# Kernel optimization log

Measured on AMD Instinct MI355X. Metric: run time of the kernel, lower is better.

The kernel has to match this reference:

```python
import jax, jax.numpy as jnp
import numpy as np

NUM_TYPES = 100
D_MODEL = 256
EPS = 1e-5


def setup_inputs() -> dict:
    key = jax.random.key(0)
    ks = jax.random.split(key, 8)
    N = 524288
    z = jax.random.randint(ks[0], (N,), 0, NUM_TYPES)
    x = jax.random.normal(ks[1], (N, 3), dtype=jnp.float32)
    emb = jax.random.normal(ks[2], (NUM_TYPES, D_MODEL), dtype=jnp.float32)
    w1 = jax.random.normal(ks[3], (3, D_MODEL), dtype=jnp.float32) * (1.0 / np.sqrt(3.0))
    b1 = jnp.zeros((D_MODEL,), dtype=jnp.float32)
    w2 = jax.random.normal(ks[4], (D_MODEL, D_MODEL), dtype=jnp.float32) * (1.0 / np.sqrt(D_MODEL))
    b2 = jnp.zeros((D_MODEL,), dtype=jnp.float32)
    gamma = jnp.ones((D_MODEL,), dtype=jnp.float32)
    beta = jnp.zeros((D_MODEL,), dtype=jnp.float32)
    return {"z": z, "x": x, "emb": emb, "w1": w1, "b1": b1,
            "w2": w2, "b2": b2, "gamma": gamma, "beta": beta}


def reference(z, x, emb, w1, b1, w2, b2, gamma, beta):
    # Embedding gather: [N, d]
    h = emb[z]
    # pos MLP: Linear(3,d) -> SiLU -> Linear(d,d)
    p = jnp.dot(x, w1) + b1
    p = jax.nn.silu(p)
    p = jnp.dot(p, w2) + b2
    h = h + p
    # LayerNorm over last dim
    mu = jnp.mean(h, axis=-1, keepdims=True)
    var = jnp.mean(jnp.square(h - mu), axis=-1, keepdims=True)
    h = (h - mu) * jax.lax.rsqrt(var + EPS) * gamma + beta
    return h
```

## Files before the change

### kernel.cpp

```cpp
#include <hip/hip_runtime.h>

#define EPS 1e-5f
#define WAVES 4

typedef __attribute__((ext_vector_type(8)))  short short8;
typedef __attribute__((ext_vector_type(4)))  short short4_t;
typedef __attribute__((ext_vector_type(16))) float f32x16;
typedef __attribute__((ext_vector_type(4)))  float f32x4;

__device__ inline unsigned f2bf(float f) {
    unsigned u = __builtin_bit_cast(unsigned, f);
    return (u + 0x7fffu + ((u >> 16) & 1u)) >> 16;
}

__global__ void prep(const float* __restrict__ w2, const float* __restrict__ emb,
                     const float* __restrict__ b2,
                     unsigned short* __restrict__ w2f, unsigned* __restrict__ embp) {
    int idx = blockIdx.x * 256 + threadIdx.x;
    if (idx < 65536) {
        int e    = idx & 7;
        int lane = (idx >> 3) & 63;
        int ks   = (idx >> 9) & 15;
        int nf   = idx >> 13;
        int k    = ks * 16 + ((lane >> 5) << 3) + e;
        int n    = nf * 32 + (lane & 31);
        w2f[idx] = (unsigned short)f2bf(w2[k * 256 + n]);
    } else if (idx < 65536 + 12800) {
        int i   = idx - 65536;
        int row = i >> 7;
        int w   = i & 127;
        int g   = w >> 5;
        int c   = w & 31;
        int clo = g * 64 + c;
        int chi = clo + 32;
        unsigned lo = f2bf(emb[row * 256 + clo] + b2[clo]);
        unsigned hi = f2bf(emb[row * 256 + chi] + b2[chi]);
        embp[i] = lo | (hi << 16);
    }
}

__global__ __launch_bounds__(256, 2) void fused_kernel(
    const int* __restrict__ z, const float* __restrict__ x,
    const float* __restrict__ w1, const float* __restrict__ b1,
    const unsigned short* __restrict__ w2f, const unsigned* __restrict__ embp,
    const float* __restrict__ gamma, const float* __restrict__ beta,
    float* __restrict__ out, int N)
{
    __shared__ char  p_lds[WAVES * 16384];
    __shared__ float x_lds[WAVES][32][4];
    __shared__ int   z_lds[WAVES][32];

    const int tid  = threadIdx.x;
    const int wave = tid >> 6;
    const int lane = tid & 63;
    const int l31  = lane & 31;
    const int h    = lane >> 5;
    char* pbuf = p_lds + wave * 16384;

    const int tiles = N >> 5;
    const int t = blockIdx.x * WAVES + wave;
    if (t >= tiles) return;
    const int R = t << 5;

    if (lane < 32) {
        int r = R + lane;
        x_lds[wave][lane][0] = x[r * 3 + 0];
        x_lds[wave][lane][1] = x[r * 3 + 1];
        x_lds[wave][lane][2] = x[r * 3 + 2];
        z_lds[wave][lane]    = z[r];
    }

    f32x16 acc[8];
#pragma unroll
    for (int j = 0; j < 16; ++j) {
        const int rl = (j & 3) + ((j >> 2) << 3) + (h << 2);
        const unsigned* er = embp + z_lds[wave][rl] * 128 + l31;
#pragma unroll
        for (int g = 0; g < 4; ++g) {
            unsigned u = er[g * 32];
            acc[2 * g][j]     = __builtin_bit_cast(float, u << 16);
            acc[2 * g + 1][j] = __builtin_bit_cast(float, u & 0xffff0000u);
        }
    }

    const int  c0  = lane * 4;
    const f32x4 w1a = *(const f32x4*)(w1 + c0);
    const f32x4 w1b = *(const f32x4*)(w1 + 256 + c0);
    const f32x4 w1c = *(const f32x4*)(w1 + 512 + c0);
    const f32x4 b1v = *(const f32x4*)(b1 + c0);
    float gv[8], bv[8];
#pragma unroll
    for (int nf = 0; nf < 8; ++nf) {
        int c = nf * 32 + l31;
        gv[nf] = gamma[c]; bv[nf] = beta[c];
    }

#pragma unroll
    for (int r = 0; r < 32; ++r) {
        float x0 = x_lds[wave][r][0];
        float x1 = x_lds[wave][r][1];
        float x2 = x_lds[wave][r][2];
        short4_t pv;
#pragma unroll
        for (int j = 0; j < 4; ++j) {
            float tv = x0 * w1a[j] + x1 * w1b[j] + x2 * w1c[j] + b1v[j];
            float s  = tv * __builtin_amdgcn_rcpf(1.f + __expf(-tv));
            pv[j] = (short)f2bf(s);
        }
        int off = (r * 512 + lane * 8) ^ ((r & 7) << 4);
        *(short4_t*)(pbuf + off) = pv;
    }

#pragma unroll
    for (int ks = 0; ks < 16; ++ks) {
        int aoff = (l31 * 512 + ks * 32 + h * 16) ^ ((l31 & 7) << 4);
        short8 a = *(const short8*)(pbuf + aoff);
        const unsigned short* bp = w2f + ks * 512 + lane * 8;
#pragma unroll
        for (int nf = 0; nf < 8; ++nf) {
            short8 b = *(const short8*)(bp + nf * 8192);
            acc[nf] = __builtin_amdgcn_mfma_f32_32x32x16_bf16(a, b, acc[nf], 0, 0, 0);
        }
    }

#pragma unroll
    for (int j = 0; j < 16; ++j) {
        const int rl = (j & 3) + ((j >> 2) << 3) + (h << 2);
        float hv[8];
        float hsum = 0.f, hsq = 0.f;
#pragma unroll
        for (int nf = 0; nf < 8; ++nf) {
            float v = acc[nf][j];
            hv[nf] = v; hsum += v; hsq += v * v;
        }
#pragma unroll
        for (int d = 1; d < 32; d <<= 1) {
            hsum += __shfl_xor(hsum, d, 64);
            hsq  += __shfl_xor(hsq,  d, 64);
        }
        float mu  = hsum * (1.f / 256.f);
        float var = hsq * (1.f / 256.f) - mu * mu;
        float rs  = rsqrtf(var + EPS);
        float* orow = out + (size_t)(R + rl) * 256 + l31;
#pragma unroll
        for (int nf = 0; nf < 8; ++nf)
            __builtin_nontemporal_store((hv[nf] - mu) * rs * gv[nf] + bv[nf],
                                        orow + nf * 32);
    }
}

extern "C" void kernel_launch(void* const* d_in, const int* in_sizes, int n_in,
                              void* d_out, int out_size, void* d_ws, size_t ws_size,
                              hipStream_t stream) {
    const int*   z     = (const int*)d_in[0];
    const float* x     = (const float*)d_in[1];
    const float* emb   = (const float*)d_in[2];
    const float* w1    = (const float*)d_in[3];
    const float* b1    = (const float*)d_in[4];
    const float* w2    = (const float*)d_in[5];
    const float* b2    = (const float*)d_in[6];
    const float* gamma = (const float*)d_in[7];
    const float* beta  = (const float*)d_in[8];
    float* out = (float*)d_out;
    const int N = in_sizes[0];

    unsigned short* w2f  = (unsigned short*)d_ws;
    unsigned*       embp = (unsigned*)((char*)d_ws + 131072);

    prep<<<(65536 + 12800 + 255) / 256, 256, 0, stream>>>(w2, emb, b2, w2f, embp);

    int tiles  = N >> 5;
    int blocks = (tiles + WAVES - 1) / WAVES;
    fused_kernel<<<blocks, 256, 0, stream>>>(z, x, w1, b1, w2f, embp,
                                             gamma, beta, out, N);
}
```

Before: 185.0 us.

## Split output columns across waves with shared 64-row A tile and cross-wave LayerNorm

The block now handles 64 rows instead of one 32-row tile per wave. Each of the four waves computes 64 output columns for all 64 rows, so the SiLU activation tile is built once in LDS and shared, and each wave loads only a quarter of W2. The accumulator count drops from 8 to 4 MFMA tiles per wave, which lowers register pressure and lets launch bounds ask for 3 blocks per CU. The cost is extra __syncthreads barriers and a cross-wave LDS reduction of the LayerNorm partial sums.

```diff
diff --git a/kernel.cpp b/kernel.cpp
--- a/kernel.cpp
+++ b/kernel.cpp
@@ -1,7 +1,6 @@
 #include <hip/hip_runtime.h>
 
 #define EPS 1e-5f
-#define WAVES 4
 
 typedef __attribute__((ext_vector_type(8)))  short short8;
 typedef __attribute__((ext_vector_type(4)))  short short4_t;
@@ -39,67 +38,66 @@
     }
 }
 
-__global__ __launch_bounds__(256, 2) void fused_kernel(
+__global__ __launch_bounds__(256, 3) void fused_kernel(
     const int* __restrict__ z, const float* __restrict__ x,
     const float* __restrict__ w1, const float* __restrict__ b1,
     const unsigned short* __restrict__ w2f, const unsigned* __restrict__ embp,
     const float* __restrict__ gamma, const float* __restrict__ beta,
     float* __restrict__ out, int N)
 {
-    __shared__ char  p_lds[WAVES * 16384];
-    __shared__ float x_lds[WAVES][32][4];
-    __shared__ int   z_lds[WAVES][32];
+    __shared__ char  a_lds[32768];
+    __shared__ float x_lds[64][4];
+    __shared__ int   z_lds[64];
+    __shared__ float part[64][4][2];
 
     const int tid  = threadIdx.x;
     const int wave = tid >> 6;
     const int lane = tid & 63;
     const int l31  = lane & 31;
     const int h    = lane >> 5;
-    char* pbuf = p_lds + wave * 16384;
+    const int l15  = lane & 15;
+    const int h4   = lane >> 4;
 
-    const int tiles = N >> 5;
-    const int t = blockIdx.x * WAVES + wave;
-    if (t >= tiles) return;
-    const int R = t << 5;
+    const int R = blockIdx.x << 6;
 
-    if (lane < 32) {
-        int r = R + lane;
-        x_lds[wave][lane][0] = x[r * 3 + 0];
-        x_lds[wave][lane][1] = x[r * 3 + 1];
-        x_lds[wave][lane][2] = x[r * 3 + 2];
-        z_lds[wave][lane]    = z[r];
+    if (tid < 64) {
+        int r = R + tid;
+        x_lds[tid][0] = x[r * 3 + 0];
+        x_lds[tid][1] = x[r * 3 + 1];
+        x_lds[tid][2] = x[r * 3 + 2];
+        z_lds[tid]    = z[r];
+    }
+    __syncthreads();
+
+    f32x16 acc[2][2];
+#pragma unroll
+    for (int rb = 0; rb < 2; ++rb)
+#pragma unroll
+    for (int j = 0; j < 16; ++j) {
+        const int row = rb * 32 + (j & 3) + ((j >> 2) << 3) + (h << 2);
+        unsigned u = embp[z_lds[row] * 128 + wave * 32 + l31];
+        acc[rb][0][j] = __builtin_bit_cast(float, u << 16);
+        acc[rb][1][j] = __builtin_bit_cast(float, u & 0xffff0000u);
     }
 
-    f32x16 acc[8];
+    float gv[2], bv[2];
 #pragma unroll
-    for (int j = 0; j < 16; ++j) {
-        const int rl = (j & 3) + ((j >> 2) << 3) + (h << 2);
-        const unsigned* er = embp + z_lds[wave][rl] * 128 + l31;
-#pragma unroll
-        for (int g = 0; g < 4; ++g) {
-            unsigned u = er[g * 32];
-            acc[2 * g][j]     = __builtin_bit_cast(float, u << 16);
-            acc[2 * g + 1][j] = __builtin_bit_cast(float, u & 0xffff0000u);
-        }
+    for (int nfi = 0; nfi < 2; ++nfi) {
+        int c = wave * 64 + nfi * 32 + l31;
+        gv[nfi] = gamma[c]; bv[nfi] = beta[c];
     }
 
-    const int  c0  = lane * 4;
+    const int  c0  = wave * 64 + l15 * 4;
     const f32x4 w1a = *(const f32x4*)(w1 + c0);
     const f32x4 w1b = *(const f32x4*)(w1 + 256 + c0);
     const f32x4 w1c = *(const f32x4*)(w1 + 512 + c0);
     const f32x4 b1v = *(const f32x4*)(b1 + c0);
-    float gv[8], bv[8];
 #pragma unroll
-    for (int nf = 0; nf < 8; ++nf) {
-        int c = nf * 32 + l31;
-        gv[nf] = gamma[c]; bv[nf] = beta[c];
-    }
-
-#pragma unroll
-    for (int r = 0; r < 32; ++r) {
-        float x0 = x_lds[wave][r][0];
-        float x1 = x_lds[wave][r][1];
-        float x2 = x_lds[wave][r][2];
+    for (int rr = 0; rr < 16; ++rr) {
+        const int row = h4 * 16 + rr;
+        float x0 = x_lds[row][0];
+        float x1 = x_lds[row][1];
+        float x2 = x_lds[row][2];
         short4_t pv;
 #pragma unroll
         for (int j = 0; j < 4; ++j) {
@@ -107,45 +105,57 @@
             float s  = tv * __builtin_amdgcn_rcpf(1.f + __expf(-tv));
             pv[j] = (short)f2bf(s);
         }
-        int off = (r * 512 + lane * 8) ^ ((r & 7) << 4);
-        *(short4_t*)(pbuf + off) = pv;
+        int off = (row * 512 + c0 * 2) ^ ((row & 7) << 4);
+        *(short4_t*)(a_lds + off) = pv;
+    }
+    __syncthreads();
+
+#pragma unroll
+    for (int ks = 0; ks < 16; ++ks) {
+        short8 a0 = *(const short8*)(a_lds + ((l31 * 512 + ks * 32 + h * 16) ^ ((l31 & 7) << 4)));
+        short8 a1 = *(const short8*)(a_lds + (((32 + l31) * 512 + ks * 32 + h * 16) ^ ((l31 & 7) << 4)));
+        const unsigned short* bp = w2f + ks * 512 + lane * 8;
+        short8 b0 = *(const short8*)(bp + (2 * wave) * 8192);
+        short8 b1f = *(const short8*)(bp + (2 * wave + 1) * 8192);
+        acc[0][0] = __builtin_amdgcn_mfma_f32_32x32x16_bf16(a0, b0,  acc[0][0], 0, 0, 0);
+        acc[0][1] = __builtin_amdgcn_mfma_f32_32x32x16_bf16(a0, b1f, acc[0][1], 0, 0, 0);
+        acc[1][0] = __builtin_amdgcn_mfma_f32_32x32x16_bf16(a1, b0,  acc[1][0], 0, 0, 0);
+        acc[1][1] = __builtin_amdgcn_mfma_f32_32x32x16_bf16(a1, b1f, acc[1][1], 0, 0, 0);
     }
 
 #pragma unroll
-    for (int ks = 0; ks < 16; ++ks) {
-        int aoff = (l31 * 512 + ks * 32 + h * 16) ^ ((l31 & 7) << 4);
-        short8 a = *(const short8*)(pbuf + aoff);
-        const unsigned short* bp = w2f + ks * 512 + lane * 8;
+    for (int rb = 0; rb < 2; ++rb)
 #pragma unroll
-        for (int nf = 0; nf < 8; ++nf) {
-            short8 b = *(const short8*)(bp + nf * 8192);
-            acc[nf] = __builtin_amdgcn_mfma_f32_32x32x16_bf16(a, b, acc[nf], 0, 0, 0);
+    for (int j = 0; j < 16; ++j) {
+        float s = acc[rb][0][j] + acc[rb][1][j];
+        float q = acc[rb][0][j] * acc[rb][0][j] + acc[rb][1][j] * acc[rb][1][j];
+#pragma unroll
+        for (int d = 1; d < 32; d <<= 1) {
+            s += __shfl_xor(s, d, 64);
+            q += __shfl_xor(q, d, 64);
         }
+        const int row = rb * 32 + (j & 3) + ((j >> 2) << 3) + (h << 2);
+        if (l31 == 0) { part[row][wave][0] = s; part[row][wave][1] = q; }
     }
+    __syncthreads();
 
 #pragma unroll
+    for (int rb = 0; rb < 2; ++rb)
+#pragma unroll
     for (int j = 0; j < 16; ++j) {
-        const int rl = (j & 3) + ((j >> 2) << 3) + (h << 2);
-        float hv[8];
-        float hsum = 0.f, hsq = 0.f;
+        const int row = rb * 32 + (j & 3) + ((j >> 2) << 3) + (h << 2);
+        f32x4 p0 = *(const f32x4*)&part[row][0][0];
+        f32x4 p1 = *(const f32x4*)&part[row][2][0];
+        float sum = p0[0] + p0[2] + p1[0] + p1[2];
+        float sq  = p0[1] + p0[3] + p1[1] + p1[3];
+        float mu  = sum * (1.f / 256.f);
+        float var = sq * (1.f / 256.f) - mu * mu;
+        float rs  = rsqrtf(var + EPS);
+        float* orow = out + (size_t)(R + row) * 256 + wave * 64 + l31;
 #pragma unroll
-        for (int nf = 0; nf < 8; ++nf) {
-            float v = acc[nf][j];
-            hv[nf] = v; hsum += v; hsq += v * v;
-        }
-#pragma unroll
-        for (int d = 1; d < 32; d <<= 1) {
-            hsum += __shfl_xor(hsum, d, 64);
-            hsq  += __shfl_xor(hsq,  d, 64);
-        }
-        float mu  = hsum * (1.f / 256.f);
-        float var = hsq * (1.f / 256.f) - mu * mu;
-        float rs  = rsqrtf(var + EPS);
-        float* orow = out + (size_t)(R + rl) * 256 + l31;
-#pragma unroll
-        for (int nf = 0; nf < 8; ++nf)
-            __builtin_nontemporal_store((hv[nf] - mu) * rs * gv[nf] + bv[nf],
-                                        orow + nf * 32);
+        for (int nfi = 0; nfi < 2; ++nfi)
+            __builtin_nontemporal_store((acc[rb][nfi][j] - mu) * rs * gv[nfi] + bv[nfi],
+                                        orow + nfi * 32);
     }
 }
 
@@ -169,8 +179,7 @@
 
     prep<<<(65536 + 12800 + 255) / 256, 256, 0, stream>>>(w2, emb, b2, w2f, embp);
 
-    int tiles  = N >> 5;
-    int blocks = (tiles + WAVES - 1) / WAVES;
+    int blocks = N >> 6;
     fused_kernel<<<blocks, 256, 0, stream>>>(z, x, w1, b1, w2f, embp,
                                              gamma, beta, out, N);
 }
```

New measurement: 223.7 us. 20.9% more time.

## Split hidden-dim SiLU and GEMM into two halves to halve LDS buffer

Applied to the files above, without the earlier changes.

The first-layer SiLU output is now produced and consumed in two 128-column halves, each followed by its 8 K-steps of MFMA, so the per-wave LDS staging buffer shrinks from 16KB to 8KB. This cuts LDS per block from 64KB to 32KB, which may allow more resident blocks per CU and lets SiLU compute of one half interleave with MFMA work. In exchange there is an extra phase boundary per tile, and occupancy may still be capped by registers (launch_bounds 256,2).

```diff
diff --git a/kernel.cpp b/kernel.cpp
--- a/kernel.cpp
+++ b/kernel.cpp
@@ -4,9 +4,8 @@
 #define WAVES 4
 
 typedef __attribute__((ext_vector_type(8)))  short short8;
-typedef __attribute__((ext_vector_type(4)))  short short4_t;
 typedef __attribute__((ext_vector_type(16))) float f32x16;
-typedef __attribute__((ext_vector_type(4)))  float f32x4;
+typedef __attribute__((ext_vector_type(2)))  float f32x2;
 
 __device__ inline unsigned f2bf(float f) {
     unsigned u = __builtin_bit_cast(unsigned, f);
@@ -46,7 +45,7 @@
     const float* __restrict__ gamma, const float* __restrict__ beta,
     float* __restrict__ out, int N)
 {
-    __shared__ char  p_lds[WAVES * 16384];
+    __shared__ char  p_lds[WAVES * 8192];
     __shared__ float x_lds[WAVES][32][4];
     __shared__ int   z_lds[WAVES][32];
 
@@ -55,7 +54,7 @@
     const int lane = tid & 63;
     const int l31  = lane & 31;
     const int h    = lane >> 5;
-    char* pbuf = p_lds + wave * 16384;
+    char* pbuf = p_lds + wave * 8192;
 
     const int tiles = N >> 5;
     const int t = blockIdx.x * WAVES + wave;
@@ -83,46 +82,45 @@
         }
     }
 
-    const int  c0  = lane * 4;
-    const f32x4 w1a = *(const f32x4*)(w1 + c0);
-    const f32x4 w1b = *(const f32x4*)(w1 + 256 + c0);
-    const f32x4 w1c = *(const f32x4*)(w1 + 512 + c0);
-    const f32x4 b1v = *(const f32x4*)(b1 + c0);
+#pragma unroll
+    for (int half = 0; half < 2; ++half) {
+        const int c = half * 128 + lane * 2;
+        const f32x2 wa = *(const f32x2*)(w1 + c);
+        const f32x2 wb = *(const f32x2*)(w1 + 256 + c);
+        const f32x2 wc = *(const f32x2*)(w1 + 512 + c);
+        const f32x2 bb = *(const f32x2*)(b1 + c);
+#pragma unroll
+        for (int r = 0; r < 32; ++r) {
+            float x0 = x_lds[wave][r][0];
+            float x1 = x_lds[wave][r][1];
+            float x2 = x_lds[wave][r][2];
+            float t0 = x0 * wa[0] + x1 * wb[0] + x2 * wc[0] + bb[0];
+            float t1 = x0 * wa[1] + x1 * wb[1] + x2 * wc[1] + bb[1];
+            float s0 = t0 * __builtin_amdgcn_rcpf(1.f + __expf(-t0));
+            float s1 = t1 * __builtin_amdgcn_rcpf(1.f + __expf(-t1));
+            unsigned pv = f2bf(s0) | (f2bf(s1) << 16);
+            int off = (r * 256 + lane * 4) ^ ((r & 7) << 4);
+            *(unsigned*)(pbuf + off) = pv;
+        }
+#pragma unroll
+        for (int ks = 0; ks < 8; ++ks) {
+            int aoff = (l31 * 256 + ks * 32 + h * 16) ^ ((l31 & 7) << 4);
+            short8 a = *(const short8*)(pbuf + aoff);
+            const unsigned short* bp = w2f + (half * 8 + ks) * 512 + lane * 8;
+#pragma unroll
+            for (int nf = 0; nf < 8; ++nf) {
+                short8 b = *(const short8*)(bp + nf * 8192);
+                acc[nf] = __builtin_amdgcn_mfma_f32_32x32x16_bf16(a, b, acc[nf], 0, 0, 0);
+            }
+        }
+    }
+
     float gv[8], bv[8];
 #pragma unroll
     for (int nf = 0; nf < 8; ++nf) {
-        int c = nf * 32 + l31;
-        gv[nf] = gamma[c]; bv[nf] = beta[c];
+        int cc = nf * 32 + l31;
+        gv[nf] = gamma[cc]; bv[nf] = beta[cc];
     }
-
-#pragma unroll
-    for (int r = 0; r < 32; ++r) {
-        float x0 = x_lds[wave][r][0];
-        float x1 = x_lds[wave][r][1];
-        float x2 = x_lds[wave][r][2];
-        short4_t pv;
-#pragma unroll
-        for (int j = 0; j < 4; ++j) {
-            float tv = x0 * w1a[j] + x1 * w1b[j] + x2 * w1c[j] + b1v[j];
-            float s  = tv * __builtin_amdgcn_rcpf(1.f + __expf(-tv));
-            pv[j] = (short)f2bf(s);
-        }
-        int off = (r * 512 + lane * 8) ^ ((r & 7) << 4);
-        *(short4_t*)(pbuf + off) = pv;
-    }
-
-#pragma unroll
-    for (int ks = 0; ks < 16; ++ks) {
-        int aoff = (l31 * 512 + ks * 32 + h * 16) ^ ((l31 & 7) << 4);
-        short8 a = *(const short8*)(pbuf + aoff);
-        const unsigned short* bp = w2f + ks * 512 + lane * 8;
-#pragma unroll
-        for (int nf = 0; nf < 8; ++nf) {
-            short8 b = *(const short8*)(bp + nf * 8192);
-            acc[nf] = __builtin_amdgcn_mfma_f32_32x32x16_bf16(a, b, acc[nf], 0, 0, 0);
-        }
-    }
-
 #pragma unroll
     for (int j = 0; j < 16; ++j) {
         const int rl = (j & 3) + ((j >> 2) << 3) + (h << 2);
```

Measured after the change: 398.8 us. 2.16x slower.
